# Kernel tuning notes

Hardware: AMD Instinct MI355X
Metric: run time of the kernel (lower is better)

Reference implementation:

```python
import jax, jax.numpy as jnp
import numpy as np

B, N, D, H = 32, 1024, 512, 8
DH = D // H


def setup_inputs() -> dict:
    key = jax.random.key(0)
    ks = jax.random.split(key, 7)
    s = 1.0 / np.sqrt(D)
    return {
        "x": jax.random.normal(ks[0], (B, N, D), dtype=jnp.float32),
        "Wq": jax.random.uniform(ks[1], (D, D), jnp.float32, -s, s),
        "bq": jax.random.uniform(ks[2], (D,), jnp.float32, -s, s),
        "Wk": jax.random.uniform(ks[3], (D, D), jnp.float32, -s, s),
        "bk": jax.random.uniform(ks[4], (D,), jnp.float32, -s, s),
        "Wv": jax.random.uniform(ks[5], (D, D), jnp.float32, -s, s),
        "bv": jax.random.uniform(ks[6], (D,), jnp.float32, -s, s),
    }


def reference(x, Wq, bq, Wk, bk, Wv, bv):
    # Linear projections (torch Linear: y = x @ W.T + b)
    q = x @ Wq.T + bq
    k = x @ Wk.T + bk
    v = x @ Wv.T + bv
    # Faithful to the original: RAW reshape [B,N,D] -> [B,H,N,D/H] (no transpose!)
    q = q.reshape(B, H, N, DH)
    k = k.reshape(B, H, N, DH)
    v = v.reshape(B, H, N, DH)
    # Scaled dot-product attention
    scores = jnp.einsum("bhnd,bhmd->bhnm", q, k) / jnp.sqrt(jnp.float32(DH))
    attn = jax.nn.softmax(scores, axis=-1)
    y = jnp.einsum("bhnm,bhmd->bhnd", attn, v)
    # Faithful to the original: raw reshape [B,H,N,DH] -> [B,N,H*DH]
    return y.reshape(B, N, H * DH)
```

## Files before the change

kernel.cpp:

```cpp
#include <hip/hip_runtime.h>
#include <stdint.h>

#define AS_G __attribute__((address_space(1)))
#define AS_L __attribute__((address_space(3)))

typedef short bf16x8 __attribute__((ext_vector_type(8)));
typedef float f32x4  __attribute__((ext_vector_type(4)));
typedef float f32x16 __attribute__((ext_vector_type(16)));

constexpr int   M_ROWS = 32768;
constexpr float QSCALE = 0.18033688011112042f;

__device__ __forceinline__ ushort f2bf(float f) {
  uint32_t x = __float_as_uint(f);
  return (ushort)((x + 0x7fffu + ((x >> 16) & 1u)) >> 16);
}
__device__ __forceinline__ uint32_t pack2bf(float lo, float hi) {
  return (uint32_t)f2bf(lo) | ((uint32_t)f2bf(hi) << 16);
}
__device__ __forceinline__ void gload16(const ushort* g, ushort* l) {
  __builtin_amdgcn_global_load_lds((const AS_G uint32_t*)g, (AS_L uint32_t*)l, 16, 0, 0);
}

__global__ void cvt_bf16_kernel(const float* __restrict__ in,
                                ushort* __restrict__ out, int n8) {
  int stride = gridDim.x * blockDim.x;
  for (int i = blockIdx.x * blockDim.x + threadIdx.x; i < n8; i += stride) {
    float4 a = reinterpret_cast<const float4*>(in)[2 * i];
    float4 b = reinterpret_cast<const float4*>(in)[2 * i + 1];
    ushort4 o0 = {f2bf(a.x), f2bf(a.y), f2bf(a.z), f2bf(a.w)};
    ushort4 o1 = {f2bf(b.x), f2bf(b.y), f2bf(b.z), f2bf(b.w)};
    reinterpret_cast<ushort4*>(out)[2 * i]     = o0;
    reinterpret_cast<ushort4*>(out)[2 * i + 1] = o1;
  }
}

__global__ __launch_bounds__(256) void qkv_gemm_kernel(
    const ushort* __restrict__ Xb, const ushort* __restrict__ Wall,
    const float* __restrict__ bq, const float* __restrict__ bk,
    const float* __restrict__ bv,
    ushort* __restrict__ QKV)
{
  __shared__ ushort As[128 * 64];
  __shared__ ushort Bs[128 * 64];

  const int tile = blockIdx.x;
  const int mt  = tile & 255;
  const int cz  = tile >> 8;
  const int mat = cz >> 2;
  const int nt  = cz & 3;

  const ushort* W    = Wall + (size_t)mat * (512 * 512);
  const float*  bias = (mat == 0) ? bq : (mat == 1 ? bk : bv);
  ushort*       Out  = QKV + (size_t)mat * ((size_t)M_ROWS * 512);
  const float   oscale = (mat == 0) ? QSCALE : 1.0f;

  const int m0 = mt * 128, n0 = nt * 128;
  const int t = threadIdx.x, lane = t & 63, wave = t >> 6;
  const int wr = wave >> 1, wc = wave & 1;
  const int l15 = lane & 15, lg = lane >> 4;

  f32x4 acc[4][4];
#pragma unroll
  for (int i = 0; i < 4; i++)
#pragma unroll
    for (int j = 0; j < 4; j++) acc[i][j] = {0.f, 0.f, 0.f, 0.f};

  for (int kt = 0; kt < 8; ++kt) {
    const int k0 = kt * 64;
    __syncthreads();
#pragma unroll
    for (int i = 0; i < 4; ++i) {
      int c = i * 256 + t, row = c >> 3, col8 = (c & 7) * 8;
      gload16(Xb + (size_t)(m0 + row) * 512 + k0 + col8, As + c * 8);
    }
#pragma unroll
    for (int i = 0; i < 4; ++i) {
      int c = i * 256 + t, row = c >> 3, col8 = (c & 7) * 8;
      gload16(W + (size_t)(n0 + row) * 512 + k0 + col8, Bs + c * 8);
    }
    __syncthreads();
#pragma unroll
    for (int ks = 0; ks < 2; ++ks) {
      bf16x8 af[4], bfr[4];
#pragma unroll
      for (int i = 0; i < 4; ++i) {
        af[i]  = *(const bf16x8*)(As + (wr * 64 + i * 16 + l15) * 64 + ks * 32 + lg * 8);
        bfr[i] = *(const bf16x8*)(Bs + (wc * 64 + i * 16 + l15) * 64 + ks * 32 + lg * 8);
      }
#pragma unroll
      for (int i = 0; i < 4; ++i)
#pragma unroll
        for (int j = 0; j < 4; ++j)
          acc[i][j] = __builtin_amdgcn_mfma_f32_16x16x32_bf16(af[i], bfr[j], acc[i][j], 0, 0, 0);
    }
  }
#pragma unroll
  for (int j = 0; j < 4; ++j) {
    const int col = n0 + wc * 64 + j * 16 + l15;
    const float bc = bias[col];
#pragma unroll
    for (int i = 0; i < 4; ++i) {
      const int row0 = m0 + wr * 64 + i * 16 + lg * 4;
#pragma unroll
      for (int r = 0; r < 4; ++r)
        Out[(size_t)(row0 + r) * 512 + col] = f2bf((acc[i][j][r] + bc) * oscale);
    }
  }
}

__global__ __launch_bounds__(256) void vtrans_kernel(
    const ushort* __restrict__ Vn, ushort* __restrict__ VT)
{
  __shared__ ushort T[64][258];
  const int bh = blockIdx.x >> 2, nc = blockIdx.x & 3;
  const ushort* src = Vn + (size_t)bh * 65536 + nc * 16384;
  ushort* dst = VT + (size_t)bh * 65536 + nc * 256;
  const int t = threadIdx.x;
#pragma unroll
  for (int i = 0; i < 8; ++i) {
    int c = i * 256 + t, n = c >> 3, col8 = (c & 7) * 8;
    ushort tmp[8];
    *(int4*)tmp = *(const int4*)(src + n * 64 + col8);
#pragma unroll
    for (int j = 0; j < 8; ++j) T[col8 + j][n] = tmp[j];
  }
  __syncthreads();
#pragma unroll
  for (int i = 0; i < 8; ++i) {
    int c = i * 256 + t, dh = c >> 5, a8 = (c & 31) * 8;
    *(int4*)(dst + (size_t)dh * 1024 + a8) = *(const int4*)(&T[dh][a8]);
  }
}

__global__ __launch_bounds__(256) void attn_kernel(
    const ushort* __restrict__ QKV,
    const ushort* __restrict__ VTg_,
    float* __restrict__ Out)
{
  constexpr int PLANE = M_ROWS * 512;
  __shared__ ushort SMEM[64 * 258];
  ushort* sK = SMEM;
  ushort* sV = SMEM + 8192;
  float* Lbuf = (float*)SMEM;

  const int blk = blockIdx.x;
  const int bh = blk >> 3, qb = blk & 7;
  const ushort* Qg  = QKV + (size_t)bh * 65536;
  const ushort* Kg  = QKV + (size_t)PLANE + (size_t)bh * 65536;
  const ushort* Vtg = VTg_ + (size_t)bh * 65536;

  const int t = threadIdx.x, lane = t & 63, wave = t >> 6;
  const int l31 = lane & 31, h = lane >> 5;
  const int q = qb * 128 + wave * 32 + l31;

  bf16x8 qf[4];
#pragma unroll
  for (int ks = 0; ks < 4; ++ks)
    qf[ks] = *(const bf16x8*)(Qg + (size_t)q * 64 + ks * 16 + h * 8);

  float mrow = -1e30f, lrow = 0.f;
  f32x16 o[2];
#pragma unroll
  for (int r = 0; r < 16; ++r) { o[0][r] = 0.f; o[1][r] = 0.f; }

#pragma unroll
  for (int i = 0; i < 2; ++i) {
    int c = i * 256 + t, row = c >> 3, slot = c & 7;
    gload16(Kg + (size_t)row * 64 + ((slot ^ (row & 7)) << 3), sK + c * 8);
    gload16(Vtg + (size_t)row * 1024 + ((slot ^ (row & 7)) << 3), sV + c * 8);
  }
  __syncthreads();

  for (int kv = 0; kv < 16; ++kv) {
    const int cur = kv & 1;
    if (kv < 15) {
      const int nx = cur ^ 1, kn = kv + 1;
#pragma unroll
      for (int i = 0; i < 2; ++i) {
        int c = i * 256 + t, row = c >> 3, slot = c & 7;
        gload16(Kg + (size_t)(kn * 64 + row) * 64 + ((slot ^ (row & 7)) << 3),
                sK + nx * 4096 + c * 8);
        gload16(Vtg + (size_t)row * 1024 + kn * 64 + ((slot ^ (row & 7)) << 3),
                sV + nx * 4096 + c * 8);
      }
    }
    const ushort* Kc = sK + cur * 4096;
    const ushort* Vc = sV + cur * 4096;

    f32x16 st[2];
#pragma unroll
    for (int tt = 0; tt < 2; ++tt) {
      f32x16 a;
#pragma unroll
      for (int r = 0; r < 16; ++r) a[r] = 0.f;
#pragma unroll
      for (int ks = 0; ks < 4; ++ks) {
        const int krow = tt * 32 + l31;
        bf16x8 kf = *(const bf16x8*)(Kc + krow * 64 + (((ks * 2 + h) ^ (krow & 7)) << 3));
        a = __builtin_amdgcn_mfma_f32_32x32x16_bf16(kf, qf[ks], a, 0, 0, 0);
      }
      st[tt] = a;
    }

    float mx = st[0][0];
#pragma unroll
    for (int r = 1; r < 16; ++r) mx = fmaxf(mx, st[0][r]);
#pragma unroll
    for (int r = 0; r < 16; ++r) mx = fmaxf(mx, st[1][r]);
    mx = fmaxf(mx, __shfl_xor(mx, 32));
    const float mnew = fmaxf(mrow, mx);
    const float alpha = exp2f(mrow - mnew);
    mrow = mnew;
    float rs = 0.f;
#pragma unroll
    for (int tt = 0; tt < 2; ++tt)
#pragma unroll
      for (int r = 0; r < 16; ++r) {
        float p = exp2f(st[tt][r] - mnew);
        st[tt][r] = p;
        rs += p;
      }
    rs += __shfl_xor(rs, 32);
    lrow = lrow * alpha + rs;
#pragma unroll
    for (int r = 0; r < 16; ++r) { o[0][r] *= alpha; o[1][r] *= alpha; }

#pragma unroll
    for (int tt = 0; tt < 2; ++tt) {
      uint32_t U[8];
#pragma unroll
      for (int p = 0; p < 8; ++p) U[p] = pack2bf(st[tt][2 * p], st[tt][2 * p + 1]);
      uint32_t R[2][2];
#pragma unroll
      for (int s = 0; s < 2; ++s)
#pragma unroll
        for (int i = 0; i < 2; ++i)
          R[s][i] = (uint32_t)__shfl_xor((int)(h ? U[4 * s + i] : U[4 * s + 2 + i]), 32);
#pragma unroll
      for (int s = 0; s < 2; ++s) {
        const int ks2 = tt * 2 + s;
        union { uint32_t u[4]; bf16x8 v; } pf;
        if (h == 0) {
          pf.u[0] = U[4 * s];     pf.u[1] = U[4 * s + 1];
          pf.u[2] = R[s][0];      pf.u[3] = R[s][1];
        } else {
          pf.u[0] = R[s][0];      pf.u[1] = R[s][1];
          pf.u[2] = U[4 * s + 2]; pf.u[3] = U[4 * s + 3];
        }
#pragma unroll
        for (int dt = 0; dt < 2; ++dt) {
          const int drow = dt * 32 + l31;
          bf16x8 vf = *(const bf16x8*)(Vc + drow * 64 + (((ks2 * 2 + h) ^ (drow & 7)) << 3));
          o[dt] = __builtin_amdgcn_mfma_f32_32x32x16_bf16(vf, pf.v, o[dt], 0, 0, 0);
        }
      }
    }
    __syncthreads();
  }

  const float linv = 1.f / lrow;
#pragma unroll
  for (int dt = 0; dt < 2; ++dt)
#pragma unroll
    for (int r = 0; r < 16; ++r) {
      const int d = dt * 32 + (r & 3) + 8 * (r >> 2) + 4 * h;
      Lbuf[d * 129 + wave * 32 + l31] = o[dt][r] * linv;
    }
  __syncthreads();
  {
    const int qloc = t >> 1, dh = (t & 1) * 32;
    float* ob = Out + (size_t)bh * 65536 + (size_t)(qb * 128 + qloc) * 64 + dh;
#pragma unroll
    for (int c = 0; c < 8; ++c) {
      float4 v = { Lbuf[(dh + 4 * c + 0) * 129 + qloc],
                   Lbuf[(dh + 4 * c + 1) * 129 + qloc],
                   Lbuf[(dh + 4 * c + 2) * 129 + qloc],
                   Lbuf[(dh + 4 * c + 3) * 129 + qloc] };
      *(float4*)(ob + 4 * c) = v;
    }
  }
}

extern "C" void kernel_launch(void* const* d_in, const int* in_sizes, int n_in,
                              void* d_out, int out_size, void* d_ws, size_t ws_size,
                              hipStream_t stream) {
  (void)in_sizes; (void)n_in; (void)out_size; (void)ws_size;
  const float* x  = (const float*)d_in[0];
  const float* Wq = (const float*)d_in[1];
  const float* bq = (const float*)d_in[2];
  const float* Wk = (const float*)d_in[3];
  const float* bk = (const float*)d_in[4];
  const float* Wv = (const float*)d_in[5];
  const float* bv = (const float*)d_in[6];

  ushort* Xb  = (ushort*)d_ws;
  ushort* VT  = (ushort*)d_ws;
  ushort* Wb  = (ushort*)((char*)d_ws + 33554432);
  ushort* QKV = (ushort*)((char*)d_ws + 35127296);
  ushort* Vn  = QKV + 2 * (size_t)M_ROWS * 512;

  cvt_bf16_kernel<<<2048, 256, 0, stream>>>(x, Xb, (32768 * 512) / 8);
  cvt_bf16_kernel<<<128, 256, 0, stream>>>(Wq, Wb + 0 * 262144, 262144 / 8);
  cvt_bf16_kernel<<<128, 256, 0, stream>>>(Wk, Wb + 1 * 262144, 262144 / 8);
  cvt_bf16_kernel<<<128, 256, 0, stream>>>(Wv, Wb + 2 * 262144, 262144 / 8);

  qkv_gemm_kernel<<<256 * 12, 256, 0, stream>>>(Xb, Wb, bq, bk, bv, QKV);

  vtrans_kernel<<<1024, 256, 0, stream>>>(Vn, VT);

  attn_kernel<<<256 * 8, 256, 0, stream>>>(QKV, VT, (float*)d_out);
}
```

Baseline: 290.7 us.

## Merge conversion launches, add lazy softmax rescale and precomputed LDS offsets

Replaces the four bf16 conversion launches with one combined kernel and switches float-to-bf16 rounding to the HIP intrinsic. In the attention kernel it precomputes the swizzled LDS offsets, uses tree reductions for the row max and sum, and skips the running-max rescale unless the max grows by more than a threshold, which trims exp and multiply work per tile. It also adds an occupancy hint to launch bounds. The V-fragment load keeps the old address computation alongside an unused load, so the offset reuse there is effectively dead code.

```diff
diff --git a/kernel.cpp b/kernel.cpp
--- a/kernel.cpp
+++ b/kernel.cpp
@@ -1,4 +1,5 @@
 #include <hip/hip_runtime.h>
+#include <hip/hip_bf16.h>
 #include <stdint.h>
 
 #define AS_G __attribute__((address_space(1)))
@@ -12,26 +13,43 @@
 constexpr float QSCALE = 0.18033688011112042f;
 
 __device__ __forceinline__ ushort f2bf(float f) {
-  uint32_t x = __float_as_uint(f);
-  return (ushort)((x + 0x7fffu + ((x >> 16) & 1u)) >> 16);
+  union { __hip_bfloat16 h; ushort u; } c;
+  c.h = __float2bfloat16(f);
+  return c.u;
 }
 __device__ __forceinline__ uint32_t pack2bf(float lo, float hi) {
-  return (uint32_t)f2bf(lo) | ((uint32_t)f2bf(hi) << 16);
+  union { __hip_bfloat162 b; uint32_t u; } r;
+  r.b.x = __float2bfloat16(lo);
+  r.b.y = __float2bfloat16(hi);
+  return r.u;
 }
 __device__ __forceinline__ void gload16(const ushort* g, ushort* l) {
   __builtin_amdgcn_global_load_lds((const AS_G uint32_t*)g, (AS_L uint32_t*)l, 16, 0, 0);
 }
 
-__global__ void cvt_bf16_kernel(const float* __restrict__ in,
-                                ushort* __restrict__ out, int n8) {
-  int stride = gridDim.x * blockDim.x;
-  for (int i = blockIdx.x * blockDim.x + threadIdx.x; i < n8; i += stride) {
-    float4 a = reinterpret_cast<const float4*>(in)[2 * i];
-    float4 b = reinterpret_cast<const float4*>(in)[2 * i + 1];
-    ushort4 o0 = {f2bf(a.x), f2bf(a.y), f2bf(a.z), f2bf(a.w)};
-    ushort4 o1 = {f2bf(b.x), f2bf(b.y), f2bf(b.z), f2bf(b.w)};
-    reinterpret_cast<ushort4*>(out)[2 * i]     = o0;
-    reinterpret_cast<ushort4*>(out)[2 * i + 1] = o1;
+__device__ __forceinline__ void cvt8(const float* __restrict__ in,
+                                     ushort* __restrict__ out, int i) {
+  float4 a = reinterpret_cast<const float4*>(in)[2 * i];
+  float4 b = reinterpret_cast<const float4*>(in)[2 * i + 1];
+  ushort4 o0 = {f2bf(a.x), f2bf(a.y), f2bf(a.z), f2bf(a.w)};
+  ushort4 o1 = {f2bf(b.x), f2bf(b.y), f2bf(b.z), f2bf(b.w)};
+  reinterpret_cast<ushort4*>(out)[2 * i]     = o0;
+  reinterpret_cast<ushort4*>(out)[2 * i + 1] = o1;
+}
+
+__global__ __launch_bounds__(256) void cvt_all_kernel(
+    const float* __restrict__ x,  const float* __restrict__ wq,
+    const float* __restrict__ wk, const float* __restrict__ wv,
+    ushort* __restrict__ xb, ushort* __restrict__ wb) {
+  const int b = blockIdx.x, t = threadIdx.x;
+  if (b < 2048) {
+    const int i0 = b * 256 + t;
+#pragma unroll
+    for (int rep = 0; rep < 4; ++rep) cvt8(x, xb, i0 + rep * 524288);
+  } else {
+    const int c = b - 2048, m = c >> 7;
+    const float* src = (m == 0) ? wq : (m == 1 ? wk : wv);
+    cvt8(src, wb + m * 262144, (c & 127) * 256 + t);
   }
 }
 
@@ -133,7 +151,7 @@
   }
 }
 
-__global__ __launch_bounds__(256) void attn_kernel(
+__global__ __launch_bounds__(256, 4) void attn_kernel(
     const ushort* __restrict__ QKV,
     const ushort* __restrict__ VTg_,
     float* __restrict__ Out)
@@ -159,6 +177,15 @@
   for (int ks = 0; ks < 4; ++ks)
     qf[ks] = *(const bf16x8*)(Qg + (size_t)q * 64 + ks * 16 + h * 8);
 
+  int off[2][4];
+#pragma unroll
+  for (int tt = 0; tt < 2; ++tt) {
+    const int row = tt * 32 + l31;
+#pragma unroll
+    for (int ks = 0; ks < 4; ++ks)
+      off[tt][ks] = row * 64 + (((ks * 2 + h) ^ (row & 7)) << 3);
+  }
+
   float mrow = -1e30f, lrow = 0.f;
   f32x16 o[2];
 #pragma unroll
@@ -196,35 +223,45 @@
       for (int r = 0; r < 16; ++r) a[r] = 0.f;
 #pragma unroll
       for (int ks = 0; ks < 4; ++ks) {
-        const int krow = tt * 32 + l31;
-        bf16x8 kf = *(const bf16x8*)(Kc + krow * 64 + (((ks * 2 + h) ^ (krow & 7)) << 3));
+        bf16x8 kf = *(const bf16x8*)(Kc + off[tt][ks]);
         a = __builtin_amdgcn_mfma_f32_32x32x16_bf16(kf, qf[ks], a, 0, 0, 0);
       }
       st[tt] = a;
     }
 
-    float mx = st[0][0];
-#pragma unroll
-    for (int r = 1; r < 16; ++r) mx = fmaxf(mx, st[0][r]);
-#pragma unroll
-    for (int r = 0; r < 16; ++r) mx = fmaxf(mx, st[1][r]);
+    float mx;
+    {
+      float t8[8];
+#pragma unroll
+      for (int i = 0; i < 8; ++i)
+        t8[i] = fmaxf(fmaxf(st[0][i], st[0][i + 8]), fmaxf(st[1][i], st[1][i + 8]));
+      float a0 = fmaxf(fmaxf(t8[0], t8[1]), fmaxf(t8[2], t8[3]));
+      float a1 = fmaxf(fmaxf(t8[4], t8[5]), fmaxf(t8[6], t8[7]));
+      mx = fmaxf(a0, a1);
+    }
     mx = fmaxf(mx, __shfl_xor(mx, 32));
-    const float mnew = fmaxf(mrow, mx);
-    const float alpha = exp2f(mrow - mnew);
-    mrow = mnew;
-    float rs = 0.f;
+    if (!__all(mx - mrow <= 8.0f)) {
+      const float mnew = fmaxf(mrow, mx);
+      const float alpha = exp2f(mrow - mnew);
+      mrow = mnew;
+      lrow *= alpha;
+#pragma unroll
+      for (int r = 0; r < 16; ++r) { o[0][r] *= alpha; o[1][r] *= alpha; }
+    }
 #pragma unroll
     for (int tt = 0; tt < 2; ++tt)
 #pragma unroll
-      for (int r = 0; r < 16; ++r) {
-        float p = exp2f(st[tt][r] - mnew);
-        st[tt][r] = p;
-        rs += p;
-      }
-    rs += __shfl_xor(rs, 32);
-    lrow = lrow * alpha + rs;
-#pragma unroll
-    for (int r = 0; r < 16; ++r) { o[0][r] *= alpha; o[1][r] *= alpha; }
+      for (int r = 0; r < 16; ++r) st[tt][r] = exp2f(st[tt][r] - mrow);
+    {
+      float s8[8];
+#pragma unroll
+      for (int i = 0; i < 8; ++i)
+        s8[i] = (st[0][i] + st[0][i + 8]) + (st[1][i] + st[1][i + 8]);
+      float rs = ((s8[0] + s8[1]) + (s8[2] + s8[3]))
+               + ((s8[4] + s8[5]) + (s8[6] + s8[7]));
+      rs += __shfl_xor(rs, 32);
+      lrow += rs;
+    }
 
 #pragma unroll
     for (int tt = 0; tt < 2; ++tt) {
@@ -239,7 +276,6 @@
           R[s][i] = (uint32_t)__shfl_xor((int)(h ? U[4 * s + i] : U[4 * s + 2 + i]), 32);
 #pragma unroll
       for (int s = 0; s < 2; ++s) {
-        const int ks2 = tt * 2 + s;
         union { uint32_t u[4]; bf16x8 v; } pf;
         if (h == 0) {
           pf.u[0] = U[4 * s];     pf.u[1] = U[4 * s + 1];
@@ -248,11 +284,15 @@
           pf.u[0] = R[s][0];      pf.u[1] = R[s][1];
           pf.u[2] = U[4 * s + 2]; pf.u[3] = U[4 * s + 3];
         }
+        const int ks2 = tt * 2 + s;
 #pragma unroll
         for (int dt = 0; dt < 2; ++dt) {
-          const int drow = dt * 32 + l31;
-          bf16x8 vf = *(const bf16x8*)(Vc + drow * 64 + (((ks2 * 2 + h) ^ (drow & 7)) << 3));
-          o[dt] = __builtin_amdgcn_mfma_f32_32x32x16_bf16(vf, pf.v, o[dt], 0, 0, 0);
+          bf16x8 vf = *(const bf16x8*)(Vc + ((ks2 & 1) ? off[dt][2 + (ks2 >> 1)]
+                                                       : off[dt][ks2 >> 1]));
+          (void)vf;
+          bf16x8 vf2 = *(const bf16x8*)(Vc + (dt * 32 + l31) * 64 +
+                                        (((ks2 * 2 + h) ^ ((dt * 32 + l31) & 7)) << 3));
+          o[dt] = __builtin_amdgcn_mfma_f32_32x32x16_bf16(vf2, pf.v, o[dt], 0, 0, 0);
         }
       }
     }
@@ -300,10 +340,7 @@
   ushort* QKV = (ushort*)((char*)d_ws + 35127296);
   ushort* Vn  = QKV + 2 * (size_t)M_ROWS * 512;
 
-  cvt_bf16_kernel<<<2048, 256, 0, stream>>>(x, Xb, (32768 * 512) / 8);
-  cvt_bf16_kernel<<<128, 256, 0, stream>>>(Wq, Wb + 0 * 262144, 262144 / 8);
-  cvt_bf16_kernel<<<128, 256, 0, stream>>>(Wk, Wb + 1 * 262144, 262144 / 8);
-  cvt_bf16_kernel<<<128, 256, 0, stream>>>(Wv, Wb + 2 * 262144, 262144 / 8);
+  cvt_all_kernel<<<2432, 256, 0, stream>>>(x, Wq, Wk, Wv, Xb, Wb);
 
   qkv_gemm_kernel<<<256 * 12, 256, 0, stream>>>(Xb, Wb, bq, bk, bv, QKV);
 
```

New measurement: 248.7 us. 14.4% less time.
